# Optimization experiments

Hardware: AMD Instinct MI355X
Metric: run time of the kernel (lower is better)

## Reference

```python
import jax, jax.numpy as jnp
import numpy as np

BATCH, C_IN, C_OUT, N_GRID, N_MODES = 64, 64, 64, 8192, 64
SCALE = 1.0 / (C_IN * C_OUT)


def setup_inputs() -> dict:
    key = jax.random.key(0)
    k1, k2, k3 = jax.random.split(key, 3)
    lhss = jax.random.normal(k1, (BATCH, C_IN, N_GRID), dtype=jnp.float32)
    # torch.rand on cfloat draws real and imag uniformly in [0,1), then scaled
    w_real = SCALE * jax.random.uniform(k2, (C_IN, C_OUT, N_MODES), dtype=jnp.float32)
    w_imag = SCALE * jax.random.uniform(k3, (C_IN, C_OUT, N_MODES), dtype=jnp.float32)
    return {"lhss": lhss, "w_real": w_real, "w_imag": w_imag}


def reference(lhss, w_real, w_imag):
    n = lhss.shape[-1]
    n_freq = n // 2 + 1  # rfft output length
    weights = w_real + 1j * w_imag  # (c_in, c_out, modes), complex64
    xf = jnp.fft.rfft(lhss)  # (b, c_in, n_freq) complex
    # complex channel-mixing on the first N_MODES frequency bins only
    mixed = jnp.einsum("bix,iox->box", xf[:, :, :N_MODES], weights)
    # zero-pad remaining high-frequency bins, then inverse rfft
    res = jnp.zeros((lhss.shape[0], weights.shape[1], n_freq), dtype=mixed.dtype)
    res = res.at[:, :, :N_MODES].set(mixed)
    return jnp.fft.irfft(res, n=n)
```

## Files before the change

### kernel.cpp

```cpp
#include <hip/hip_runtime.h>
#include <hip/hip_bf16.h>

#define NG 8192
#define NB 64
#define CI 64
#define CO 64
#define NM 64
#define NFJ 128
#define NROWS 4096

typedef __bf16 bf16x8 __attribute__((ext_vector_type(8)));
typedef float f32x4 __attribute__((ext_vector_type(4)));
typedef float f32x2 __attribute__((ext_vector_type(2)));

#define GLOAD_LDS16(gsrc, ldst)                                                   \
    __builtin_amdgcn_global_load_lds(                                             \
        (const __attribute__((address_space(1))) void*)(gsrc),                    \
        (__attribute__((address_space(3))) void*)(ldst), 16, 0, 0)


__global__ __launch_bounds__(256) void sc_prep(const float* __restrict__ wr,
                                               const float* __restrict__ wi,
                                               __bf16* __restrict__ Ft,
                                               __bf16* __restrict__ Ginv,
                                               __bf16* __restrict__ Wtf) {
    const float W0 = 6.2831853071795864769f / (float)NG;
    if (blockIdx.x < 8192) {
        int idx = blockIdx.x * 256 + threadIdx.x;
        if (idx < 128 * NG) {
            int j = idx >> 13, pos = idx & (NG - 1);
            int blk = pos >> 6, g = (pos >> 3) & 7, e = pos & 7;
            int ksrc = (blk << 6) + (((g ^ (j & 7)) << 3) | e);
            int m = j >> 1;
            int t = (m * ksrc) & (NG - 1);
            float s, c;
            __sincosf((float)t * W0, &s, &c);
            Ft[idx] = (__bf16)((j & 1) ? -s : c);
        } else {
            int i2 = idx - 128 * NG;
            int n = i2 >> 7, pos = i2 & 127;
            int g = pos >> 3, e = pos & 7;
            int psrc = ((g ^ (n & 15)) << 3) | e;
            int m = psrc >> 1, im = psrc & 1;
            int t = (m * n) & (NG - 1);
            float s, c;
            __sincosf((float)t * W0, &s, &c);
            float v;
            if (im) v = (m == 0) ? 0.0f : (-2.0f / NG) * s;
            else    v = ((m == 0) ? 1.0f : 2.0f) / NG * c;
            Ginv[i2] = (__bf16)v;
        }
    } else {
        const int i = blockIdx.x - 8192, t = threadIdx.x;
        const int o = t & 63, kq = t >> 6;
        float wrk[16], wik[16];
        const float* pr = wr + ((size_t)i * 64 + o) * 64 + kq * 16;
        const float* pq = wi + ((size_t)i * 64 + o) * 64 + kq * 16;
        #pragma unroll
        for (int m = 0; m < 4; ++m) {
            float4 a = *(const float4*)(pr + m * 4);
            float4 b = *(const float4*)(pq + m * 4);
            wrk[m*4+0]=a.x; wrk[m*4+1]=a.y; wrk[m*4+2]=a.z; wrk[m*4+3]=a.w;
            wik[m*4+0]=b.x; wik[m*4+1]=b.y; wik[m*4+2]=b.z; wik[m*4+3]=b.w;
        }
        const int ks_a = i >> 5, ks_b = 2 + (i >> 5);
        const int kg = (i >> 3) & 3, e = i & 7, ot = o >> 4, l = o & 15;
        const int pos = (kg * 16 + l) * 8 + e;
        #pragma unroll
        for (int kk = 0; kk < 16; ++kk) {
            int k = kq * 16 + kk;
            Wtf[(size_t)(((k*2+0)*4+ks_a)*4+ot)*512 + pos] = (__bf16)wrk[kk];
            Wtf[(size_t)(((k*2+0)*4+ks_b)*4+ot)*512 + pos] = (__bf16)(-wik[kk]);
            Wtf[(size_t)(((k*2+1)*4+ks_a)*4+ot)*512 + pos] = (__bf16)wik[kk];
            Wtf[(size_t)(((k*2+1)*4+ks_b)*4+ot)*512 + pos] = (__bf16)wrk[kk];
        }
    }
}

__global__ __launch_bounds__(256) void sc_dft(const float* __restrict__ A,
                                              const __bf16* __restrict__ Ft,
                                              float* __restrict__ XFp,
                                              int nsteps) {
    __shared__ __align__(16) char smem[49152];
    char* A0 = smem;
    char* A1 = smem + 8192;
    char* F0 = smem + 16384;
    char* F1 = smem + 32768;

    const int tid = threadIdx.x;
    const int w = tid >> 6, lane = tid & 63;
    const int l15 = lane & 15, kg = lane >> 4;
    const int wm = w >> 1, wn = w & 1;
    const int rt = blockIdx.x & 63, sp = blockIdx.x >> 6;
    const int r0 = rt * 64;
    const size_t kb0 = (size_t)sp * nsteps * 64;
    const int swz = l15 & 7;

    float4 av[4];
    f32x4 acc[2][4] = {};

    auto issueA = [&](int step) {
        size_t kb = kb0 + (size_t)step * 64;
        #pragma unroll
        for (int s = 0; s < 4; ++s) {
            int c = s * 256 + tid;
            av[s] = *(const float4*)(A + (size_t)(r0 + (c >> 4)) * NG + kb + (c & 15) * 4);
        }
    };
    auto writeA = [&](char* Ab) {
        #pragma unroll
        for (int s = 0; s < 4; ++s) {
            int c = s * 256 + tid, row = c >> 4, cq = c & 15;
            union { __bf16 h[4]; uint2 u; } cv;
            cv.h[0] = (__bf16)av[s].x; cv.h[1] = (__bf16)av[s].y;
            cv.h[2] = (__bf16)av[s].z; cv.h[3] = (__bf16)av[s].w;
            *(uint2*)(Ab + row * 128 + (((cq >> 1) ^ (row & 7)) << 4) + ((cq & 1) << 3)) = cv.u;
        }
    };
    auto stageF = [&](int step, char* Fb) {
        size_t kb = kb0 + (size_t)step * 64;
        #pragma unroll
        for (int s = 0; s < 4; ++s) {
            int cc = s * 256 + tid;
            GLOAD_LDS16(Ft + (size_t)(cc >> 3) * NG + kb + (cc & 7) * 8, Fb + cc * 16);
        }
    };
    auto compute = [&](const char* Ab, const char* Fb) {
        #pragma unroll
        for (int ks2 = 0; ks2 < 2; ++ks2) {
            bf16x8 a[2], b[4];
            #pragma unroll
            for (int mt = 0; mt < 2; ++mt)
                a[mt] = *(const bf16x8*)(Ab + (wm*32 + mt*16 + l15) * 128 +
                                         (((ks2*4 + kg) ^ swz) << 4));
            #pragma unroll
            for (int jt = 0; jt < 4; ++jt)
                b[jt] = *(const bf16x8*)(Fb + (wn*64 + jt*16 + l15) * 128 +
                                         (((ks2*4 + kg) ^ swz) << 4));
            #pragma unroll
            for (int mt = 0; mt < 2; ++mt)
                #pragma unroll
                for (int jt = 0; jt < 4; ++jt)
                    acc[mt][jt] = __builtin_amdgcn_mfma_f32_16x16x32_bf16(
                        a[mt], b[jt], acc[mt][jt], 0, 0, 0);
        }
    };

    issueA(0); stageF(0, F0); writeA(A0);
    __syncthreads();
    for (int t = 0; t < nsteps; ++t) {
        char* Ac = (t & 1) ? A1 : A0;
        char* Fc = (t & 1) ? F1 : F0;
        char* An = (t & 1) ? A0 : A1;
        char* Fn = (t & 1) ? F0 : F1;
        if (t + 1 < nsteps) { issueA(t + 1); stageF(t + 1, Fn); }
        compute(Ac, Fc);
        if (t + 1 < nsteps) writeA(An);
        __syncthreads();
    }
    #pragma unroll
    for (int mt = 0; mt < 2; ++mt)
        #pragma unroll
        for (int jt = 0; jt < 4; ++jt)
            #pragma unroll
            for (int rr = 0; rr < 4; ++rr)
                XFp[((size_t)sp * NROWS + r0 + wm*32 + mt*16 + kg*4 + rr) * NFJ +
                    wn*64 + jt*16 + l15] = acc[mt][jt][rr];
}

__global__ __launch_bounds__(256) void sc_red(const float* __restrict__ XFp,
                                              float* __restrict__ XF, int nsplit) {
    size_t idx = (size_t)blockIdx.x * 256 + threadIdx.x;
    f32x4 s = {};
    for (int p = 0; p < nsplit; ++p)
        s += *(const f32x4*)(XFp + (size_t)p * (NROWS * NFJ) + idx * 4);
    *(f32x4*)(XF + idx * 4) = s;
}

__global__ __launch_bounds__(256) void sc_mix(const float* __restrict__ XF,
                                              const __bf16* __restrict__ Wtf,
                                              __bf16* __restrict__ M2) {
    __shared__ __align__(16) char at[4096];
    const int t = threadIdx.x;
    const int k = blockIdx.x >> 2, bq = blockIdx.x & 3;
    const int lane = t & 63, ot = t >> 6;
    const int l15 = lane & 15, kg = lane >> 4;

    #pragma unroll
    for (int s = 0; s < 4; ++s) {
        int idx = s * 256 + t;
        int bl = idx >> 6, i = idx & 63;
        f32x2 x = *(const f32x2*)(XF + ((size_t)(bq*16 + bl) * CI + i) * NFJ + 2 * k);
        unsigned short hr = __builtin_bit_cast(unsigned short, (__bf16)x[0]);
        unsigned short hi = __builtin_bit_cast(unsigned short, (__bf16)x[1]);
        ((unsigned short*)at)[(bl*256 + (((i>>3) ^ bl) << 4) + (i&7)*2) >> 1] = hr;
        ((unsigned short*)at)[(bl*256 + ((((64+i)>>3) ^ bl) << 4) + (i&7)*2) >> 1] = hi;
    }
    __syncthreads();

    bf16x8 a[4];
    #pragma unroll
    for (int ks = 0; ks < 4; ++ks)
        a[ks] = *(const bf16x8*)(at + l15*256 + (((ks*4 + kg) ^ l15) << 4));

    f32x4 accR = {}, accI = {};
    #pragma unroll
    for (int ks = 0; ks < 4; ++ks) {
        bf16x8 b0 = *(const bf16x8*)(Wtf + (size_t)(((k*2+0)*4+ks)*4+ot)*512 + lane*8);
        accR = __builtin_amdgcn_mfma_f32_16x16x32_bf16(a[ks], b0, accR, 0, 0, 0);
    }
    #pragma unroll
    for (int ks = 0; ks < 4; ++ks) {
        bf16x8 b1 = *(const bf16x8*)(Wtf + (size_t)(((k*2+1)*4+ks)*4+ot)*512 + lane*8);
        accI = __builtin_amdgcn_mfma_f32_16x16x32_bf16(a[ks], b1, accI, 0, 0, 0);
    }
    #pragma unroll
    for (int rr = 0; rr < 4; ++rr) {
        int bg = bq*16 + kg*4 + rr;
        size_t r = (size_t)bg * CO + ot*16 + l15;
        ushort2 pk;
        pk.x = __builtin_bit_cast(unsigned short, (__bf16)accR[rr]);
        pk.y = __builtin_bit_cast(unsigned short, (__bf16)accI[rr]);
        *(ushort2*)(M2 + r * NFJ + 2 * k) = pk;
    }
}

__global__ __launch_bounds__(512) void sc_idft(const __bf16* __restrict__ M2,
                                               const __bf16* __restrict__ Ginv,
                                               float* __restrict__ out) {
    __shared__ __align__(16) char gls[32768];
    const int tid = threadIdx.x;
    const int w = tid >> 6, lane = tid & 63;
    const int l15 = lane & 15, kg = lane >> 4;
    const int wm = w >> 1;
    const int wn = w & 1;
    const int r0 = (blockIdx.x >> 6) * 128;
    const int n0 = (blockIdx.x & 63) * 128;

    #pragma unroll
    for (int s = 0; s < 4; ++s) {
        int cc = s * 512 + tid;
        GLOAD_LDS16(Ginv + (size_t)n0 * NFJ + cc * 8, gls + cc * 16);
    }

    bf16x8 af[2][4];
    #pragma unroll
    for (int mt = 0; mt < 2; ++mt)
        #pragma unroll
        for (int ks = 0; ks < 4; ++ks)
            af[mt][ks] = *(const bf16x8*)(M2 + (size_t)(r0 + wm*32 + mt*16 + l15) * NFJ +
                                          ks*32 + kg*8);
    __syncthreads();

    f32x4 acc[2][4] = {};
    #pragma unroll
    for (int nt = 0; nt < 4; ++nt) {
        int row = wn*64 + nt*16 + l15;
        bf16x8 bfr[4];
        #pragma unroll
        for (int ks = 0; ks < 4; ++ks)
            bfr[ks] = *(const bf16x8*)(gls + row * 256 + (((ks*4 + kg) ^ (row & 15)) << 4));
        #pragma unroll
        for (int mt = 0; mt < 2; ++mt)
            #pragma unroll
            for (int ks = 0; ks < 4; ++ks)
                acc[mt][nt] = __builtin_amdgcn_mfma_f32_16x16x32_bf16(
                    af[mt][ks], bfr[ks], acc[mt][nt], 0, 0, 0);
    }
    #pragma unroll
    for (int mt = 0; mt < 2; ++mt)
        #pragma unroll
        for (int nt = 0; nt < 4; ++nt)
            #pragma unroll
            for (int rr = 0; rr < 4; ++rr)
                out[(size_t)(r0 + wm*32 + mt*16 + kg*4 + rr) * NG +
                    n0 + wn*64 + nt*16 + l15] = acc[mt][nt][rr];
}

extern "C" void kernel_launch(void* const* d_in, const int* in_sizes, int n_in,
                              void* d_out, int out_size, void* d_ws, size_t ws_size,
                              hipStream_t stream) {
    const float* lhss = (const float*)d_in[0];
    const float* w_real = (const float*)d_in[1];
    const float* w_imag = (const float*)d_in[2];
    float* out = (float*)d_out;

    char* ws = (char*)d_ws;
    __bf16* Ft_sw   = (__bf16*)ws;
    __bf16* Ginv_sw = (__bf16*)(ws + (2u << 20));
    float*  XF      = (float*) (ws + (4u << 20));
    __bf16* M2      = (__bf16*)(ws + (6u << 20));
    __bf16* Wtf     = (__bf16*)(ws + (7u << 20));
    float*  XFp     = (float*) (ws + (9u << 20));

    int split;
    if      (ws_size >= (25u << 20)) split = 8;
    else if (ws_size >= (17u << 20)) split = 4;
    else if (ws_size >= (13u << 20)) split = 2;
    else                             split = 1;
    int nsteps = 128 / split;

    sc_prep<<<8256, 256, 0, stream>>>(w_real, w_imag, Ft_sw, Ginv_sw, Wtf);
    sc_dft<<<64 * split, 256, 0, stream>>>(lhss, Ft_sw, XFp, nsteps);
    sc_red<<<512, 256, 0, stream>>>(XFp, XF, split);
    sc_mix<<<256, 256, 0, stream>>>(XF, Wtf, M2);
    sc_idft<<<2048, 512, 0, stream>>>(M2, Ginv_sw, out);
}
```

Measured before the change: 95.86 us.

## Fuse split-K reduction into mix kernel with transposed partial layout

The DFT kernel now writes its split partial sums in a transposed (frequency-major) layout using vector stores, and the separate reduction kernel is removed. The mix kernel sums the split partials directly while loading its tile, converts them to bf16 and writes packed 16-byte values into shared memory. This saves one kernel launch and a round trip through the intermediate XF buffer. In exchange, the mix kernel does more global reads per block, and the DFT stores now stride by NROWS.

```diff
diff --git a/kernel.cpp b/kernel.cpp
--- a/kernel.cpp
+++ b/kernel.cpp
@@ -11,7 +11,6 @@
 
 typedef __bf16 bf16x8 __attribute__((ext_vector_type(8)));
 typedef float f32x4 __attribute__((ext_vector_type(4)));
-typedef float f32x2 __attribute__((ext_vector_type(2)));
 
 #define GLOAD_LDS16(gsrc, ldst)                                                   \
     __builtin_amdgcn_global_load_lds(                                             \
@@ -162,39 +161,46 @@
     for (int mt = 0; mt < 2; ++mt)
         #pragma unroll
         for (int jt = 0; jt < 4; ++jt)
-            #pragma unroll
-            for (int rr = 0; rr < 4; ++rr)
-                XFp[((size_t)sp * NROWS + r0 + wm*32 + mt*16 + kg*4 + rr) * NFJ +
-                    wn*64 + jt*16 + l15] = acc[mt][jt][rr];
-}
-
-__global__ __launch_bounds__(256) void sc_red(const float* __restrict__ XFp,
-                                              float* __restrict__ XF, int nsplit) {
-    size_t idx = (size_t)blockIdx.x * 256 + threadIdx.x;
-    f32x4 s = {};
-    for (int p = 0; p < nsplit; ++p)
-        s += *(const f32x4*)(XFp + (size_t)p * (NROWS * NFJ) + idx * 4);
-    *(f32x4*)(XF + idx * 4) = s;
-}
-
-__global__ __launch_bounds__(256) void sc_mix(const float* __restrict__ XF,
+            *(f32x4*)(XFp + ((size_t)sp * NFJ + wn*64 + jt*16 + l15) * NROWS +
+                      (r0 + wm*32 + mt*16 + kg*4)) = acc[mt][jt];
+}
+
+__global__ __launch_bounds__(256) void sc_mix(const float* __restrict__ XFp,
                                               const __bf16* __restrict__ Wtf,
-                                              __bf16* __restrict__ M2) {
+                                              __bf16* __restrict__ M2, int nsplit) {
     __shared__ __align__(16) char at[4096];
     const int t = threadIdx.x;
     const int k = blockIdx.x >> 2, bq = blockIdx.x & 3;
     const int lane = t & 63, ot = t >> 6;
     const int l15 = lane & 15, kg = lane >> 4;
 
-    #pragma unroll
-    for (int s = 0; s < 4; ++s) {
-        int idx = s * 256 + t;
-        int bl = idx >> 6, i = idx & 63;
-        f32x2 x = *(const f32x2*)(XF + ((size_t)(bq*16 + bl) * CI + i) * NFJ + 2 * k);
-        unsigned short hr = __builtin_bit_cast(unsigned short, (__bf16)x[0]);
-        unsigned short hi = __builtin_bit_cast(unsigned short, (__bf16)x[1]);
-        ((unsigned short*)at)[(bl*256 + (((i>>3) ^ bl) << 4) + (i&7)*2) >> 1] = hr;
-        ((unsigned short*)at)[(bl*256 + ((((64+i)>>3) ^ bl) << 4) + (i&7)*2) >> 1] = hi;
+    const int c = t >> 7, t127 = t & 127;
+    f32x4 s0 = {}, s1 = {};
+    {
+        const float* src = XFp + (size_t)(2*k + c) * NROWS + bq*1024 + t127*8;
+        const size_t pstride = (size_t)NFJ * NROWS;
+        if (nsplit == 8) {
+            #pragma unroll
+            for (int p = 0; p < 8; ++p) {
+                s0 += *(const f32x4*)(src + p*pstride);
+                s1 += *(const f32x4*)(src + p*pstride + 4);
+            }
+        } else {
+            for (int p = 0; p < nsplit; ++p) {
+                s0 += *(const f32x4*)(src + p*pstride);
+                s1 += *(const f32x4*)(src + p*pstride + 4);
+            }
+        }
+    }
+    {
+        const int bl = t127 >> 3;
+        const int i0 = (t127 & 7) * 8;
+        union { __bf16 h[8]; uint4 u; } cv;
+        cv.h[0]=(__bf16)s0[0]; cv.h[1]=(__bf16)s0[1];
+        cv.h[2]=(__bf16)s0[2]; cv.h[3]=(__bf16)s0[3];
+        cv.h[4]=(__bf16)s1[0]; cv.h[5]=(__bf16)s1[1];
+        cv.h[6]=(__bf16)s1[2]; cv.h[7]=(__bf16)s1[3];
+        *(uint4*)(at + bl*256 + ((((c*64 + i0) >> 3) ^ bl) << 4)) = cv.u;
     }
     __syncthreads();
 
@@ -288,7 +294,6 @@
     char* ws = (char*)d_ws;
     __bf16* Ft_sw   = (__bf16*)ws;
     __bf16* Ginv_sw = (__bf16*)(ws + (2u << 20));
-    float*  XF      = (float*) (ws + (4u << 20));
     __bf16* M2      = (__bf16*)(ws + (6u << 20));
     __bf16* Wtf     = (__bf16*)(ws + (7u << 20));
     float*  XFp     = (float*) (ws + (9u << 20));
@@ -302,7 +307,6 @@
 
     sc_prep<<<8256, 256, 0, stream>>>(w_real, w_imag, Ft_sw, Ginv_sw, Wtf);
     sc_dft<<<64 * split, 256, 0, stream>>>(lhss, Ft_sw, XFp, nsteps);
-    sc_red<<<512, 256, 0, stream>>>(XFp, XF, split);
-    sc_mix<<<256, 256, 0, stream>>>(XF, Wtf, M2);
+    sc_mix<<<256, 256, 0, stream>>>(XFp, Wtf, M2, split);
     sc_idft<<<2048, 512, 0, stream>>>(M2, Ginv_sw, out);
 }
```

After: 88.42 us. 7.8% less time.
